# Performance work log

Hardware: AMD Instinct MI355X
Metric: run time of the kernel (lower is better)

## Reference

```python
import jax, jax.numpy as jnp
import numpy as np

B, S, HID = 4, 2048, 1024
NH, HD = 16, 64  # op_heads, head_size (hidden_size // total_heads)
EPS = 1e-6


def setup_inputs() -> dict:
    key = jax.random.key(0)
    k1, k2, k3, k4 = jax.random.split(key, 4)
    return {
        "hidden_states": jax.random.normal(k1, (B, S, HID), dtype=jnp.float32),
        "assoc_hc_attn": jax.random.uniform(k2, (B, S, S), dtype=jnp.float32),
        "broad_hc_attn": jax.random.uniform(k3, (B, S, S), dtype=jnp.float32),
        "Wv": jax.random.normal(k4, (HID, NH * HD), dtype=jnp.float32) * 0.02,
        "bv": jnp.zeros((NH * HD,), dtype=jnp.float32),
    }


def reference(hidden_states, assoc_hc_attn, broad_hc_attn, Wv, bv):
    # v_proj + split heads -> [B, NH, S, HD]
    value = hidden_states @ Wv + bv
    sp_value = value.reshape(B, S, NH, HD).transpose(0, 2, 1, 3)

    # broad_heads == 0, so attn_heads == assoc_hc_attn broadcast over all op_heads.
    attn = assoc_hc_attn.astype(jnp.float32)  # [B, S, S]
    causal = jnp.tril(jnp.ones((S, S), dtype=bool))
    attn = jnp.where(causal, attn, 0.0)
    # sum-normalize along keys (no softmax)
    attn = attn / (EPS + attn.sum(axis=-1, keepdims=True))

    # shared attn across heads: contract once -> [B, NH, S, HD]
    out = jnp.einsum('bqk,bhkd->bhqd', attn, sp_value)
    # merge heads -> [B, S, NH*HD]
    return out.transpose(0, 2, 1, 3).reshape(B, S, NH * HD)
```

## Files before the change

kernel.cpp:

```cpp
#include <hip/hip_runtime.h>

#define B_    4
#define S_    2048
#define HID_  1024
#define NO_   1024
#define EPS_  1e-6f
#define M1_   (B_ * S_)

typedef __attribute__((ext_vector_type(8))) short  short8;
typedef __attribute__((ext_vector_type(4))) float  f32x4;
typedef unsigned short ushort_t;

__device__ __forceinline__ unsigned short f2bf(float f) {
  union { float f; unsigned int u; } v; v.f = f;
  unsigned int r = v.u + 0x7FFFu + ((v.u >> 16) & 1u);
  return (unsigned short)(r >> 16);
}
__device__ __forceinline__ unsigned pack2(float a, float b) {
  return (unsigned)f2bf(a) | ((unsigned)f2bf(b) << 16);
}

typedef __attribute__((address_space(1))) const void GASV;
typedef __attribute__((address_space(3))) void LASV;
__device__ __forceinline__ void gld16(const void* g, void* l) {
  __builtin_amdgcn_global_load_lds((GASV*)g, (LASV*)l, 16, 0, 0);
}

__global__ void k_twv(const float* __restrict__ Wv, ushort_t* __restrict__ WvT) {
  __shared__ float tile[32][33];
  int k0 = blockIdx.x * 32;
  int n0 = blockIdx.y * 32;
  int tx = threadIdx.x, ty = threadIdx.y;
  for (int i = ty; i < 32; i += 8)
    tile[i][tx] = Wv[(size_t)(k0 + i) * NO_ + n0 + tx];
  __syncthreads();
  for (int i = ty; i < 32; i += 8)
    WvT[(size_t)(n0 + i) * HID_ + k0 + tx] = f2bf(tile[tx][i]);
}

__global__ __launch_bounds__(256) void k_cvtH(const float* __restrict__ H,
                                              ushort_t* __restrict__ Hb) {
  size_t i = ((size_t)blockIdx.x * 256 + threadIdx.x) * 4;
  float4 v = *(const float4*)(H + i);
  uint2 p; p.x = pack2(v.x, v.y); p.y = pack2(v.z, v.w);
  *(uint2*)(Hb + i) = p;
}

__global__ __launch_bounds__(256) void k_prepA(const float* __restrict__ A,
                                               ushort_t* __restrict__ Ab) {
  int row  = blockIdx.x * 4 + (threadIdx.x >> 6);
  int lane = threadIdx.x & 63;
  int q = row & 2047;
  const float* rp = A + (size_t)row * S_;
  float s = 0.f;
  for (int k = lane * 4; k <= q; k += 256) {
    float4 v = *(const float4*)(rp + k);
    s += v.x;
    if (k + 1 <= q) s += v.y;
    if (k + 2 <= q) s += v.z;
    if (k + 3 <= q) s += v.w;
  }
  for (int off = 1; off < 64; off <<= 1) s += __shfl_xor(s, off, 64);
  float inv = 1.0f / (EPS_ + s);
  int wend = ((q >> 7) + 1) << 7;
  ushort_t* op = Ab + (size_t)row * S_;
  for (int k = lane * 4; k < wend; k += 256) {
    float4 v = *(const float4*)(rp + k);
    float x0 = (k + 0 <= q) ? v.x * inv : 0.f;
    float x1 = (k + 1 <= q) ? v.y * inv : 0.f;
    float x2 = (k + 2 <= q) ? v.z * inv : 0.f;
    float x3 = (k + 3 <= q) ? v.w * inv : 0.f;
    uint2 p; p.x = pack2(x0, x1); p.y = pack2(x2, x3);
    *(uint2*)(op + k) = p;
  }
}

__global__ __launch_bounds__(256) void k_vt(
    const ushort_t* __restrict__ WvT, const ushort_t* __restrict__ Hb,
    const float* __restrict__ bv, ushort_t* __restrict__ Vt) {
  __shared__ __align__(16) ushort_t lds_a[128 * 32];
  __shared__ __align__(16) ushort_t lds_b[128 * 32];
  int m0 = blockIdx.x * 128;
  int n0 = blockIdx.y * 128;
  int tid = threadIdx.x;
  int wave = tid >> 6, lane = tid & 63;
  int wr = wave >> 1, wc = wave & 1;
  int lq = lane >> 4, lm = lane & 15;

  int sr = wave * 16 + (lane >> 2);
  int sc = (lane & 3) ^ ((sr >> 1) & 3);
  const ushort_t* gA0 = WvT + (size_t)(n0 + sr) * HID_ + sc * 8;
  const ushort_t* gA1 = gA0 + (size_t)64 * HID_;
  const ushort_t* gB0 = Hb + (size_t)(m0 + sr) * HID_ + sc * 8;
  const ushort_t* gB1 = gB0 + (size_t)64 * HID_;
  char* la = (char*)lds_a;
  char* lb = (char*)lds_b;
  unsigned wslot = wave * 1024;
  int swz = (lm >> 1) & 3;

  f32x4 acc[4][4];
  for (int i = 0; i < 4; i++) for (int j = 0; j < 4; j++) acc[i][j] = (f32x4)0.0f;

  for (int it = 0; it < HID_ / 32; it++) {
    gld16(gA0, la + wslot);        gld16(gA1, la + 4096 + wslot);
    gld16(gB0, lb + wslot);        gld16(gB1, lb + 4096 + wslot);
    gA0 += 32; gA1 += 32; gB0 += 32; gB1 += 32;
    __syncthreads();
    short8 af[4], bfr[4];
#pragma unroll
    for (int mi = 0; mi < 4; mi++)
      af[mi] = *(const short8*)(la + (wr * 64 + mi * 16 + lm) * 64 + ((lq ^ swz) << 4));
#pragma unroll
    for (int ni = 0; ni < 4; ni++)
      bfr[ni] = *(const short8*)(lb + (wc * 64 + ni * 16 + lm) * 64 + ((lq ^ swz) << 4));
#pragma unroll
    for (int mi = 0; mi < 4; mi++)
#pragma unroll
      for (int ni = 0; ni < 4; ni++)
        acc[mi][ni] = __builtin_amdgcn_mfma_f32_16x16x32_bf16(af[mi], bfr[ni], acc[mi][ni], 0, 0, 0);
    __syncthreads();
  }
  for (int mi = 0; mi < 4; mi++) {
    for (int r = 0; r < 4; r++) {
      int n = n0 + wr * 64 + mi * 16 + lq * 4 + r;
      float bias = bv[n];
      for (int ni = 0; ni < 4; ni++) {
        int m = m0 + wc * 64 + ni * 16 + lm;
        int b = m >> 11;
        int s = m & 2047;
        Vt[((size_t)b * NO_ + n) * S_ + s] = f2bf(acc[mi][ni][r] + bias);
      }
    }
  }
}

__global__ __launch_bounds__(256) void k_attn(
    const ushort_t* __restrict__ Ab, const ushort_t* __restrict__ Vt,
    float* __restrict__ out) {
  __shared__ __align__(16) ushort_t lds_a[128 * 32];
  __shared__ __align__(16) ushort_t lds_b[128 * 32];
  int n0 = (blockIdx.x & 7) * 128;
  int b  = blockIdx.x >> 3;
  int q0 = (15 - (int)blockIdx.y) * 128;
  int tid = threadIdx.x;
  int wave = tid >> 6, lane = tid & 63;
  int wr = wave >> 1, wc = wave & 1;
  int lq = lane >> 4, lm = lane & 15;

  int sr = wave * 16 + (lane >> 2);
  int sc = (lane & 3) ^ ((sr >> 1) & 3);
  const ushort_t* gA0 = Ab + ((size_t)(b * S_ + q0 + sr)) * S_ + sc * 8;
  const ushort_t* gA1 = gA0 + (size_t)64 * S_;
  const ushort_t* gB0 = Vt + ((size_t)(b * NO_ + n0 + sr)) * S_ + sc * 8;
  const ushort_t* gB1 = gB0 + (size_t)64 * S_;
  char* la = (char*)lds_a;
  char* lb = (char*)lds_b;
  unsigned wslot = wave * 1024;
  int swz = (lm >> 1) & 3;

  f32x4 acc[4][4];
  for (int i = 0; i < 4; i++) for (int j = 0; j < 4; j++) acc[i][j] = (f32x4)0.0f;

  const int iters = (q0 >> 5) + 4;
  for (int it = 0; it < iters; it++) {
    gld16(gA0, la + wslot);        gld16(gA1, la + 4096 + wslot);
    gld16(gB0, lb + wslot);        gld16(gB1, lb + 4096 + wslot);
    gA0 += 32; gA1 += 32; gB0 += 32; gB1 += 32;
    __syncthreads();
    short8 af[4], bfr[4];
#pragma unroll
    for (int mi = 0; mi < 4; mi++)
      af[mi] = *(const short8*)(la + (wr * 64 + mi * 16 + lm) * 64 + ((lq ^ swz) << 4));
#pragma unroll
    for (int ni = 0; ni < 4; ni++)
      bfr[ni] = *(const short8*)(lb + (wc * 64 + ni * 16 + lm) * 64 + ((lq ^ swz) << 4));
#pragma unroll
    for (int mi = 0; mi < 4; mi++)
#pragma unroll
      for (int ni = 0; ni < 4; ni++)
        acc[mi][ni] = __builtin_amdgcn_mfma_f32_16x16x32_bf16(af[mi], bfr[ni], acc[mi][ni], 0, 0, 0);
    __syncthreads();
  }
  for (int mi = 0; mi < 4; mi++) {
    for (int r = 0; r < 4; r++) {
      int q = q0 + wr * 64 + mi * 16 + lq * 4 + r;
      for (int ni = 0; ni < 4; ni++) {
        int n = n0 + wc * 64 + ni * 16 + lm;
        out[((size_t)b * S_ + q) * NO_ + n] = acc[mi][ni][r];
      }
    }
  }
}

extern "C" void kernel_launch(void* const* d_in, const int* in_sizes, int n_in,
                              void* d_out, int out_size, void* d_ws, size_t ws_size,
                              hipStream_t stream) {
  const float* H  = (const float*)d_in[0];
  const float* A  = (const float*)d_in[1];
  const float* Wv = (const float*)d_in[3];
  const float* bv = (const float*)d_in[4];
  float* out = (float*)d_out;

  char* ws = (char*)d_ws;
  ushort_t* WvT = (ushort_t*)ws;
  ushort_t* Hb  = (ushort_t*)(ws + 2097152);
  ushort_t* Vt  = (ushort_t*)(ws + 2097152 + 16777216);
  ushort_t* Abf = (ushort_t*)(ws + 2097152 + 2 * 16777216);

  k_twv  <<<dim3(HID_ / 32, NO_ / 32), dim3(32, 8), 0, stream>>>(Wv, WvT);
  k_cvtH <<<(M1_ * HID_) / (256 * 4), 256, 0, stream>>>(H, Hb);
  k_prepA<<<M1_ / 4, 256, 0, stream>>>(A, Abf);
  k_vt   <<<dim3(M1_ / 128, NO_ / 128), 256, 0, stream>>>(WvT, Hb, bv, Vt);
  k_attn <<<dim3(32, 16), 256, 0, stream>>>(Abf, Vt, out);
}
```

Before: 251.9 us.

## Halve GEMM tiles to 128x64 with two waves and cache rows in prepA

```diff
diff --git a/kernel.cpp b/kernel.cpp
--- a/kernel.cpp
+++ b/kernel.cpp
@@ -51,68 +51,79 @@
   int row  = blockIdx.x * 4 + (threadIdx.x >> 6);
   int lane = threadIdx.x & 63;
   int q = row & 2047;
+  int wend = ((q >> 7) + 1) << 7;
   const float* rp = A + (size_t)row * S_;
+  float4 v[8];
   float s = 0.f;
-  for (int k = lane * 4; k <= q; k += 256) {
-    float4 v = *(const float4*)(rp + k);
-    s += v.x;
-    if (k + 1 <= q) s += v.y;
-    if (k + 2 <= q) s += v.z;
-    if (k + 3 <= q) s += v.w;
+#pragma unroll
+  for (int i = 0; i < 8; i++) {
+    int k = i * 256 + lane * 4;
+    if (k < wend) {
+      float4 t = *(const float4*)(rp + k);
+      t.x = (k + 0 <= q) ? t.x : 0.f;
+      t.y = (k + 1 <= q) ? t.y : 0.f;
+      t.z = (k + 2 <= q) ? t.z : 0.f;
+      t.w = (k + 3 <= q) ? t.w : 0.f;
+      v[i] = t;
+      s += t.x + t.y + t.z + t.w;
+    }
   }
   for (int off = 1; off < 64; off <<= 1) s += __shfl_xor(s, off, 64);
   float inv = 1.0f / (EPS_ + s);
-  int wend = ((q >> 7) + 1) << 7;
   ushort_t* op = Ab + (size_t)row * S_;
-  for (int k = lane * 4; k < wend; k += 256) {
-    float4 v = *(const float4*)(rp + k);
-    float x0 = (k + 0 <= q) ? v.x * inv : 0.f;
-    float x1 = (k + 1 <= q) ? v.y * inv : 0.f;
-    float x2 = (k + 2 <= q) ? v.z * inv : 0.f;
-    float x3 = (k + 3 <= q) ? v.w * inv : 0.f;
-    uint2 p; p.x = pack2(x0, x1); p.y = pack2(x2, x3);
-    *(uint2*)(op + k) = p;
-  }
-}
-
-__global__ __launch_bounds__(256) void k_vt(
+#pragma unroll
+  for (int i = 0; i < 8; i++) {
+    int k = i * 256 + lane * 4;
+    if (k < wend) {
+      uint2 p;
+      p.x = pack2(v[i].x * inv, v[i].y * inv);
+      p.y = pack2(v[i].z * inv, v[i].w * inv);
+      *(uint2*)(op + k) = p;
+    }
+  }
+}
+
+__global__ __launch_bounds__(128) void k_vt(
     const ushort_t* __restrict__ WvT, const ushort_t* __restrict__ Hb,
     const float* __restrict__ bv, ushort_t* __restrict__ Vt) {
-  __shared__ __align__(16) ushort_t lds_a[128 * 32];
+  __shared__ __align__(16) ushort_t lds_a[64 * 32];
   __shared__ __align__(16) ushort_t lds_b[128 * 32];
   int m0 = blockIdx.x * 128;
-  int n0 = blockIdx.y * 128;
+  int n0 = blockIdx.y * 64;
   int tid = threadIdx.x;
   int wave = tid >> 6, lane = tid & 63;
-  int wr = wave >> 1, wc = wave & 1;
   int lq = lane >> 4, lm = lane & 15;
 
-  int sr = wave * 16 + (lane >> 2);
-  int sc = (lane & 3) ^ ((sr >> 1) & 3);
-  const ushort_t* gA0 = WvT + (size_t)(n0 + sr) * HID_ + sc * 8;
-  const ushort_t* gA1 = gA0 + (size_t)64 * HID_;
-  const ushort_t* gB0 = Hb + (size_t)(m0 + sr) * HID_ + sc * 8;
-  const ushort_t* gB1 = gB0 + (size_t)64 * HID_;
+  int rr = lane >> 2;
+  int sc = (lane & 3) ^ ((rr >> 1) & 3);
+  const ushort_t* gA = WvT + (size_t)(n0 + wave * 32 + rr) * HID_ + sc * 8;
+  const ushort_t* gB = Hb  + (size_t)(m0 + wave * 64 + rr) * HID_ + sc * 8;
   char* la = (char*)lds_a;
   char* lb = (char*)lds_b;
-  unsigned wslot = wave * 1024;
+  char* la_w = la + wave * 2048;
+  char* lb_w = lb + wave * 4096;
   int swz = (lm >> 1) & 3;
+  int fo = (lq ^ swz) << 4;
 
   f32x4 acc[4][4];
   for (int i = 0; i < 4; i++) for (int j = 0; j < 4; j++) acc[i][j] = (f32x4)0.0f;
 
   for (int it = 0; it < HID_ / 32; it++) {
-    gld16(gA0, la + wslot);        gld16(gA1, la + 4096 + wslot);
-    gld16(gB0, lb + wslot);        gld16(gB1, lb + 4096 + wslot);
-    gA0 += 32; gA1 += 32; gB0 += 32; gB1 += 32;
+    gld16(gA,               la_w);
+    gld16(gA + 16 * HID_,   la_w + 1024);
+    gld16(gB,               lb_w);
+    gld16(gB + 16 * HID_,   lb_w + 1024);
+    gld16(gB + 32 * HID_,   lb_w + 2048);
+    gld16(gB + 48 * HID_,   lb_w + 3072);
+    gA += 32; gB += 32;
     __syncthreads();
     short8 af[4], bfr[4];
 #pragma unroll
     for (int mi = 0; mi < 4; mi++)
-      af[mi] = *(const short8*)(la + (wr * 64 + mi * 16 + lm) * 64 + ((lq ^ swz) << 4));
+      af[mi] = *(const short8*)(la + (mi * 16 + lm) * 64 + fo);
 #pragma unroll
     for (int ni = 0; ni < 4; ni++)
-      bfr[ni] = *(const short8*)(lb + (wc * 64 + ni * 16 + lm) * 64 + ((lq ^ swz) << 4));
+      bfr[ni] = *(const short8*)(lb + (wave * 64 + ni * 16 + lm) * 64 + fo);
 #pragma unroll
     for (int mi = 0; mi < 4; mi++)
 #pragma unroll
@@ -122,10 +133,10 @@
   }
   for (int mi = 0; mi < 4; mi++) {
     for (int r = 0; r < 4; r++) {
-      int n = n0 + wr * 64 + mi * 16 + lq * 4 + r;
+      int n = n0 + mi * 16 + lq * 4 + r;
       float bias = bv[n];
       for (int ni = 0; ni < 4; ni++) {
-        int m = m0 + wc * 64 + ni * 16 + lm;
+        int m = m0 + wave * 64 + ni * 16 + lm;
         int b = m >> 11;
         int s = m & 2047;
         Vt[((size_t)b * NO_ + n) * S_ + s] = f2bf(acc[mi][ni][r] + bias);
@@ -134,46 +145,51 @@
   }
 }
 
-__global__ __launch_bounds__(256) void k_attn(
+__global__ __launch_bounds__(128) void k_attn(
     const ushort_t* __restrict__ Ab, const ushort_t* __restrict__ Vt,
     float* __restrict__ out) {
   __shared__ __align__(16) ushort_t lds_a[128 * 32];
-  __shared__ __align__(16) ushort_t lds_b[128 * 32];
-  int n0 = (blockIdx.x & 7) * 128;
-  int b  = blockIdx.x >> 3;
-  int q0 = (15 - (int)blockIdx.y) * 128;
+  __shared__ __align__(16) ushort_t lds_b[64 * 32];
+  int col = blockIdx.x;
+  int n0 = (col & 15) * 64;
+  int b  = col >> 4;
+  int t  = 15 - (int)blockIdx.y;
+  int q0 = t * 128;
   int tid = threadIdx.x;
   int wave = tid >> 6, lane = tid & 63;
-  int wr = wave >> 1, wc = wave & 1;
   int lq = lane >> 4, lm = lane & 15;
 
-  int sr = wave * 16 + (lane >> 2);
-  int sc = (lane & 3) ^ ((sr >> 1) & 3);
-  const ushort_t* gA0 = Ab + ((size_t)(b * S_ + q0 + sr)) * S_ + sc * 8;
-  const ushort_t* gA1 = gA0 + (size_t)64 * S_;
-  const ushort_t* gB0 = Vt + ((size_t)(b * NO_ + n0 + sr)) * S_ + sc * 8;
-  const ushort_t* gB1 = gB0 + (size_t)64 * S_;
+  int rr = lane >> 2;
+  int sc = (lane & 3) ^ ((rr >> 1) & 3);
+  const ushort_t* gA = Ab + ((size_t)(b * S_ + q0 + wave * 64 + rr)) * S_ + sc * 8;
+  const ushort_t* gB = Vt + ((size_t)(b * NO_ + n0 + wave * 32 + rr)) * S_ + sc * 8;
   char* la = (char*)lds_a;
   char* lb = (char*)lds_b;
-  unsigned wslot = wave * 1024;
+  char* la_w = la + wave * 4096;
+  char* lb_w = lb + wave * 2048;
   int swz = (lm >> 1) & 3;
+  int fo = (lq ^ swz) << 4;
 
   f32x4 acc[4][4];
   for (int i = 0; i < 4; i++) for (int j = 0; j < 4; j++) acc[i][j] = (f32x4)0.0f;
 
   const int iters = (q0 >> 5) + 4;
   for (int it = 0; it < iters; it++) {
-    gld16(gA0, la + wslot);        gld16(gA1, la + 4096 + wslot);
-    gld16(gB0, lb + wslot);        gld16(gB1, lb + 4096 + wslot);
-    gA0 += 32; gA1 += 32; gB0 += 32; gB1 += 32;
+    gld16(gA,             la_w);
+    gld16(gA + 16 * S_,   la_w + 1024);
+    gld16(gA + 32 * S_,   la_w + 2048);
+    gld16(gA + 48 * S_,   la_w + 3072);
+    gld16(gB,             lb_w);
+    gld16(gB + 16 * S_,   lb_w + 1024);
+    gA += 32; gB += 32;
     __syncthreads();
     short8 af[4], bfr[4];
 #pragma unroll
     for (int mi = 0; mi < 4; mi++)
-      af[mi] = *(const short8*)(la + (wr * 64 + mi * 16 + lm) * 64 + ((lq ^ swz) << 4));
+      af[mi] = *(const short8*)(la + (wave * 64 + mi * 16 + lm) * 64 + fo);
 #pragma unroll
     for (int ni = 0; ni < 4; ni++)
-      bfr[ni] = *(const short8*)(lb + (wc * 64 + ni * 16 + lm) * 64 + ((lq ^ swz) << 4));
+      bfr[ni] = *(const short8*)(lb + (ni * 16 + lm) * 64 + fo);
 #pragma unroll
     for (int mi = 0; mi < 4; mi++)
 #pragma unroll
@@ -183,9 +199,9 @@
   }
   for (int mi = 0; mi < 4; mi++) {
     for (int r = 0; r < 4; r++) {
-      int q = q0 + wr * 64 + mi * 16 + lq * 4 + r;
+      int q = q0 + wave * 64 + mi * 16 + lq * 4 + r;
       for (int ni = 0; ni < 4; ni++) {
-        int n = n0 + wc * 64 + ni * 16 + lm;
+        int n = n0 + ni * 16 + lm;
         out[((size_t)b * S_ + q) * NO_ + n] = acc[mi][ni][r];
       }
     }
@@ -210,6 +226,6 @@
   k_twv  <<<dim3(HID_ / 32, NO_ / 32), dim3(32, 8), 0, stream>>>(Wv, WvT);
   k_cvtH <<<(M1_ * HID_) / (256 * 4), 256, 0, stream>>>(H, Hb);
   k_prepA<<<M1_ / 4, 256, 0, stream>>>(A, Abf);
-  k_vt   <<<dim3(M1_ / 128, NO_ / 128), 256, 0, stream>>>(WvT, Hb, bv, Vt);
-  k_attn <<<dim3(32, 16), 256, 0, stream>>>(Abf, Vt, out);
-}
+  k_vt   <<<dim3(M1_ / 128, NO_ / 64), 128, 0, stream>>>(WvT, Hb, bv, Vt);
+  k_attn <<<dim3(64, 16), 128, 0, stream>>>(Abf, Vt, out);
+}
```

Result: faster. 245.1 us (-2.7%).
